# Optimization experiments

Hardware: AMD Instinct MI355X
Metric: run time of the kernel (lower is better)

Reference implementation:

```python
import jax, jax.numpy as jnp
import numpy as np

V, H, B, T = 8192, 1024, 64, 128

def setup_inputs() -> dict:
    key = jax.random.key(0)
    ks = jax.random.split(key, 7)
    s = 1.0 / np.sqrt(H)                     # torch LSTMCell/Linear default init bound
    xg = np.sqrt(6.0 / (H + V))              # xavier_uniform for fc_out.weight
    return {
        "h0":   jax.random.normal(ks[0], (B, H), jnp.float32),
        "W_ih": jax.random.uniform(ks[1], (4 * H, V), jnp.float32, -s, s),
        "W_hh": jax.random.uniform(ks[2], (4 * H, H), jnp.float32, -s, s),
        "b_ih": jax.random.uniform(ks[3], (4 * H,), jnp.float32, -s, s),
        "b_hh": jax.random.uniform(ks[4], (4 * H,), jnp.float32, -s, s),
        "W_fc": jax.random.uniform(ks[5], (V, H), jnp.float32, -xg, xg),
        "b_fc": jax.random.uniform(ks[6], (V,), jnp.float32, -s, s),
        "max_length": T,
    }

def reference(h0, W_ih, W_hh, b_ih, b_hh, W_fc, b_fc, max_length):
    B_, H_ = h0.shape
    V_ = W_ih.shape[1]
    # hidden state fed to the cell is ALWAYS features[1] (h0) in the original code,
    # so its contribution to the gates is constant across timesteps.
    hh = h0 @ W_hh.T + b_hh + b_ih  # (B, 4H)

    def step(carry, _):
        x, c = carry                          # x: (B,V) accumulated one-hots, c: (B,H)
        gates = x @ W_ih.T + hh               # (B, 4H), torch gate order i,f,g,o
        i, f, g, o = jnp.split(gates, 4, axis=1)
        c = jax.nn.sigmoid(f) * c + jax.nn.sigmoid(i) * jnp.tanh(g)
        h = jax.nn.sigmoid(o) * jnp.tanh(c)
        out = h @ W_fc.T + b_fc               # (B, V)
        idx = jnp.argmax(out, axis=1)
        x = x + jax.nn.one_hot(idx, V_, dtype=x.dtype)  # +1 at argmax (cumulative)
        return (x, c), out

    init = (jnp.zeros((B_, V_), h0.dtype), jnp.zeros((B_, H_), h0.dtype))
    _, outs = jax.lax.scan(step, init, None, length=max_length)  # (T, B, V)
    return jnp.transpose(outs, (1, 2, 0))  # (B, V, T)
```

## Files before the change

kernel.cpp:

```cpp
#include <hip/hip_runtime.h>
#include <math.h>

#define VDIM 8192
#define HDIM 1024
#define BDIM 64
#define TDIM 128
#define H4   4096
#define TCH  16
#define NFC  512
#define GS   1088

__device__ __forceinline__ float sigf(float x){ return 1.0f/(1.0f + expf(-x)); }

__device__ __forceinline__ unsigned long long packmax(float v, int vidx){
    unsigned int u = __float_as_uint(v);
    u = (u & 0x80000000u) ? ~u : (u | 0x80000000u);
    return ((unsigned long long)u << 32) | (unsigned int)(VDIM - 1 - vidx);
}

__global__ void __launch_bounds__(256)
hh_kernel(const float* __restrict__ h0, const float* __restrict__ W_hh,
          const float* __restrict__ b_ih, const float* __restrict__ b_hh,
          float* __restrict__ gates)
{
    int blk = blockIdx.x;
    int b = blk >> 4;
    int j = (blk & 15)*256 + threadIdx.x;
    const float* hr = h0 + (size_t)b*HDIM;
    const float* wr = W_hh + (size_t)j*HDIM;
    float s = 0.f;
    for (int k = 0; k < HDIM; k += 4){
        float4 hv = *(const float4*)(hr + k);
        float4 wv = *(const float4*)(wr + k);
        s = fmaf(hv.x, wv.x, s); s = fmaf(hv.y, wv.y, s);
        s = fmaf(hv.z, wv.z, s); s = fmaf(hv.w, wv.w, s);
    }
    gates[(size_t)b*H4 + j] = s + b_ih[j] + b_hh[j];
}

__global__ void __launch_bounds__(256)
cell0_kernel(const float* __restrict__ gates, float* __restrict__ cbuf,
             float* __restrict__ hbuf)
{
    int b = blockIdx.x, u = threadIdx.x*4;
    const float* gb = gates + (size_t)b*H4;
    float4 gi = *(const float4*)(gb + u);
    float4 gf = *(const float4*)(gb + 1024 + u);
    float4 gg = *(const float4*)(gb + 2048 + u);
    float4 go = *(const float4*)(gb + 3072 + u);
    (void)gf;
    float4 c4, h4;
    c4.x = sigf(gi.x)*tanhf(gg.x); c4.y = sigf(gi.y)*tanhf(gg.y);
    c4.z = sigf(gi.z)*tanhf(gg.z); c4.w = sigf(gi.w)*tanhf(gg.w);
    h4.x = sigf(go.x)*tanhf(c4.x); h4.y = sigf(go.y)*tanhf(c4.y);
    h4.z = sigf(go.z)*tanhf(c4.z); h4.w = sigf(go.w)*tanhf(c4.w);
    *(float4*)(cbuf + (size_t)b*HDIM + u) = c4;
    *(float4*)(hbuf + (size_t)b*HDIM + u) = h4;
}

__global__ void __launch_bounds__(256)
tr_kernel(const float* __restrict__ W, float* __restrict__ WT)
{
    __shared__ float tile[64][65];
    const int jb = blockIdx.x * 64;
    const int vb = blockIdx.y * 64;
    const int tx = threadIdx.x & 63;
    const int ty = threadIdx.x >> 6;
    #pragma unroll
    for (int k = 0; k < 64; k += 4)
        tile[ty + k][tx] = W[(size_t)(jb + ty + k)*VDIM + vb + tx];
    __syncthreads();
    #pragma unroll
    for (int k = 0; k < 64; k += 4)
        WT[(size_t)(vb + ty + k)*H4 + jb + tx] = tile[tx][ty + k];
}

__global__ void __launch_bounds__(512, 4)
fc_kernel(const float* __restrict__ W_fc, const float* __restrict__ b_fc,
          const float* __restrict__ hbuf, float* __restrict__ out,
          float* __restrict__ stage,
          unsigned long long* __restrict__ pmax, int t)
{
    __shared__ float buf[16*GS];
    __shared__ unsigned long long bmax[256];
    const int tid = threadIdx.x;
    const int blk = blockIdx.x;
    const int vbase = blk * 16;
    const int g  = tid >> 5;
    const int s  = tid & 31;
    const int b0 = (s >> 2) * 8;
    const int v0 = (s & 3) * 4;
    const int k0 = g * 64;

    float acc[8][4];
    #pragma unroll
    for (int i=0;i<8;++i){
        #pragma unroll
        for (int j=0;j<4;++j) acc[i][j] = 0.f;
    }

    const float* hb = hbuf + (size_t)b0*HDIM + k0;
    const float* wb = W_fc + (size_t)(vbase + v0)*HDIM + k0;

    #pragma unroll 2
    for (int kc = 0; kc < 16; ++kc){
        float4 h4[8], w4[4];
        #pragma unroll
        for (int i=0;i<8;++i) h4[i] = *(const float4*)(hb + (size_t)i*HDIM + kc*4);
        #pragma unroll
        for (int j=0;j<4;++j) w4[j] = *(const float4*)(wb + (size_t)j*HDIM + kc*4);
        #pragma unroll
        for (int i=0;i<8;++i){
            #pragma unroll
            for (int j=0;j<4;++j){
                acc[i][j] = fmaf(h4[i].x, w4[j].x, acc[i][j]);
                acc[i][j] = fmaf(h4[i].y, w4[j].y, acc[i][j]);
                acc[i][j] = fmaf(h4[i].z, w4[j].z, acc[i][j]);
                acc[i][j] = fmaf(h4[i].w, w4[j].w, acc[i][j]);
            }
        }
    }

    {
        float* bp = buf + g*GS;
        #pragma unroll
        for (int i=0;i<8;++i){
            #pragma unroll
            for (int j=0;j<4;++j) bp[(b0+i)*17 + v0 + j] = acc[i][j];
        }
    }
    __syncthreads();

    if (tid < 256){
        const int eb = tid >> 2;
        const int vv = (tid & 3) * 4;
        float4 rr[16];
        #pragma unroll
        for (int q=0;q<16;++q){
            const float* bp = buf + q*GS + eb*17 + vv;
            rr[q].x = bp[0]; rr[q].y = bp[1]; rr[q].z = bp[2]; rr[q].w = bp[3];
        }
        #pragma unroll
        for (int half = 8; half >= 1; half >>= 1){
            #pragma unroll
            for (int i=0;i<8;++i){
                if (i < half){
                    rr[i].x += rr[i+half].x; rr[i].y += rr[i+half].y;
                    rr[i].z += rr[i+half].z; rr[i].w += rr[i+half].w;
                }
            }
        }
        float4 r = rr[0];
        const int v = vbase + vv;
        r.x += b_fc[v]; r.y += b_fc[v+1]; r.z += b_fc[v+2]; r.w += b_fc[v+3];
        if (stage){
            *(float4*)(stage + (((size_t)(t & (TCH-1))*BDIM + eb)*VDIM + v)) = r;
        } else {
            float* ob = out + ((size_t)eb*VDIM + v)*TDIM + t;
            ob[0] = r.x; ob[TDIM] = r.y; ob[2*TDIM] = r.z; ob[3*TDIM] = r.w;
        }
        unsigned long long m  = packmax(r.x, v);
        unsigned long long m2 = packmax(r.y, v+1); if (m2 > m) m = m2;
        m2 = packmax(r.z, v+2); if (m2 > m) m = m2;
        m2 = packmax(r.w, v+3); if (m2 > m) m = m2;
        bmax[tid] = m;
    }
    __syncthreads();
    if (tid < 64){
        unsigned long long mm = bmax[tid*4];
        #pragma unroll
        for (int q=1;q<4;++q){ unsigned long long z = bmax[tid*4+q]; if (z > mm) mm = z; }
        pmax[(size_t)tid*NFC + blk] = mm;
    }
}

__global__ void __launch_bounds__(256)
flush_kernel(const float* __restrict__ stage, float* __restrict__ out, int t0)
{
    const size_t n = (size_t)blockIdx.x*256 + threadIdx.x;
    const int b = (int)(n >> 13);
    const int v = (int)(n & (VDIM-1));
    const size_t st = (size_t)BDIM*VDIM;
    const float* sp = stage + (size_t)b*VDIM + v;
    float* op = out + ((size_t)b*VDIM + v)*TDIM + t0;
    float4 o0, o1, o2, o3;
    o0.x = sp[0*st];  o0.y = sp[1*st];  o0.z = sp[2*st];  o0.w = sp[3*st];
    o1.x = sp[4*st];  o1.y = sp[5*st];  o1.z = sp[6*st];  o1.w = sp[7*st];
    o2.x = sp[8*st];  o2.y = sp[9*st];  o2.z = sp[10*st]; o2.w = sp[11*st];
    o3.x = sp[12*st]; o3.y = sp[13*st]; o3.z = sp[14*st]; o3.w = sp[15*st];
    *(float4*)(op + 0)  = o0;
    *(float4*)(op + 4)  = o1;
    *(float4*)(op + 8)  = o2;
    *(float4*)(op + 12) = o3;
}

__global__ void __launch_bounds__(256)
cell_kernel(const float* __restrict__ W_ih, const float* __restrict__ W_ihT,
            float* __restrict__ gates, float* __restrict__ cbuf,
            float* __restrict__ hbuf, const unsigned long long* __restrict__ pmax)
{
    __shared__ float gbuf[H4];
    __shared__ unsigned long long red[256];
    const int b = blockIdx.x, tid = threadIdx.x;

    {
        unsigned long long a = pmax[(size_t)b*NFC + tid];
        unsigned long long c = pmax[(size_t)b*NFC + tid + 256];
        red[tid] = (c > a) ? c : a;
    }
    __syncthreads();
    for (int st = 128; st; st >>= 1){
        if (tid < st){ if (red[tid+st] > red[tid]) red[tid] = red[tid+st]; }
        __syncthreads();
    }
    const int idx = VDIM - 1 - (int)(unsigned int)(red[0] & 0xffffffffULL);

    float* gb = gates + (size_t)b*H4;
    if (W_ihT){
        const float* row = W_ihT + (size_t)idx*H4;
        #pragma unroll
        for (int q = 0; q < 4; ++q){
            int j4 = q*1024 + tid*4;
            float4 wv = *(const float4*)(row + j4);
            float4 gv = *(const float4*)(gb + j4);
            gv.x += wv.x; gv.y += wv.y; gv.z += wv.z; gv.w += wv.w;
            *(float4*)(gb + j4) = gv;
            *(float4*)(gbuf + j4) = gv;
        }
    } else {
        #pragma unroll
        for (int q = 0; q < 16; ++q){
            int j = q*256 + tid;
            float gv = gb[j] + W_ih[(size_t)j*VDIM + idx];
            gb[j] = gv;
            gbuf[j] = gv;
        }
    }
    __syncthreads();

    int u = tid*4;
    float4 gi = *(float4*)(gbuf + u);
    float4 gf = *(float4*)(gbuf + 1024 + u);
    float4 gg = *(float4*)(gbuf + 2048 + u);
    float4 go = *(float4*)(gbuf + 3072 + u);
    float4 c4 = *(float4*)(cbuf + (size_t)b*HDIM + u);
    c4.x = sigf(gf.x)*c4.x + sigf(gi.x)*tanhf(gg.x);
    c4.y = sigf(gf.y)*c4.y + sigf(gi.y)*tanhf(gg.y);
    c4.z = sigf(gf.z)*c4.z + sigf(gi.z)*tanhf(gg.z);
    c4.w = sigf(gf.w)*c4.w + sigf(gi.w)*tanhf(gg.w);
    float4 h4;
    h4.x = sigf(go.x)*tanhf(c4.x); h4.y = sigf(go.y)*tanhf(c4.y);
    h4.z = sigf(go.z)*tanhf(c4.z); h4.w = sigf(go.w)*tanhf(c4.w);
    *(float4*)(cbuf + (size_t)b*HDIM + u) = c4;
    *(float4*)(hbuf + (size_t)b*HDIM + u) = h4;
}

extern "C" void kernel_launch(void* const* d_in, const int* in_sizes, int n_in,
                              void* d_out, int out_size, void* d_ws, size_t ws_size,
                              hipStream_t stream)
{
    const float* h0   = (const float*)d_in[0];
    const float* W_ih = (const float*)d_in[1];
    const float* W_hh = (const float*)d_in[2];
    const float* b_ih = (const float*)d_in[3];
    const float* b_hh = (const float*)d_in[4];
    const float* W_fc = (const float*)d_in[5];
    const float* b_fc = (const float*)d_in[6];
    float* out = (float*)d_out;

    float* gates = (float*)d_ws;
    float* cbuf  = gates + (size_t)BDIM*H4;
    float* hbuf  = cbuf  + (size_t)BDIM*HDIM;
    unsigned long long* pmax = (unsigned long long*)(hbuf + (size_t)BDIM*HDIM);

    size_t off = (size_t)BDIM*H4*4 + 2*(size_t)BDIM*HDIM*4 + (size_t)BDIM*NFC*8;
    const size_t STAGE_B = (size_t)TCH*BDIM*VDIM*4;
    const size_t WT_B    = (size_t)VDIM*H4*4;
    float* stage = nullptr;
    float* wT    = nullptr;
    if (ws_size >= off + STAGE_B){ stage = (float*)((char*)d_ws + off); off += STAGE_B; }
    if (ws_size >= off + WT_B)   { wT    = (float*)((char*)d_ws + off); off += WT_B; }

    hipLaunchKernelGGL(hh_kernel, dim3(1024), dim3(256), 0, stream,
                       h0, W_hh, b_ih, b_hh, gates);
    hipLaunchKernelGGL(cell0_kernel, dim3(64), dim3(256), 0, stream,
                       gates, cbuf, hbuf);
    if (wT){
        hipLaunchKernelGGL(tr_kernel, dim3(64, 128), dim3(256), 0, stream,
                           W_ih, wT);
    }

    for (int t = 0; t < TDIM; ++t){
        hipLaunchKernelGGL(fc_kernel, dim3(NFC), dim3(512), 0, stream,
                           W_fc, b_fc, hbuf, out, stage, pmax, t);
        if (stage && (t & (TCH-1)) == (TCH-1)){
            hipLaunchKernelGGL(flush_kernel, dim3(BDIM*VDIM/256), dim3(256), 0, stream,
                               stage, out, t - (TCH-1));
        }
        if (t < TDIM - 1){
            hipLaunchKernelGGL(cell_kernel, dim3(64), dim3(256), 0, stream,
                               W_ih, wT, gates, cbuf, hbuf, pmax);
        }
    }
}
```

Measured before the change: 7.987 ms.

## Split FC kernel across batch halves and widen cell kernel grid

The FC kernel now splits the batch into two halves, launching 1024 blocks that each compute 32 batch rows by 16 vocab entries, which halves per-thread register accumulators and doubles grid parallelism. The cell step, when the transposed W_ih is available, becomes a 256-block kernel of single wavefronts. Each block redoes the argmax reduction with wave shuffles and handles a quarter of the hidden units, so no shared memory or block syncs are needed. The trade-off is that h and W tiles are loaded twice across batch halves and the argmax reduction is repeated four times per batch row.

```diff
diff --git a/kernel.cpp b/kernel.cpp
--- a/kernel.cpp
+++ b/kernel.cpp
@@ -8,7 +8,7 @@
 #define H4   4096
 #define TCH  16
 #define NFC  512
-#define GS   1088
+#define GS2  544
 
 __device__ __forceinline__ float sigf(float x){ return 1.0f/(1.0f + expf(-x)); }
 
@@ -81,20 +81,23 @@
           float* __restrict__ stage,
           unsigned long long* __restrict__ pmax, int t)
 {
-    __shared__ float buf[16*GS];
-    __shared__ unsigned long long bmax[256];
+    __shared__ float buf[16*GS2];
+    __shared__ unsigned long long bmax[128];
     const int tid = threadIdx.x;
     const int blk = blockIdx.x;
-    const int vbase = blk * 16;
+    const int bh  = blk >> 9;
+    const int vt  = blk & 511;
+    const int vbase = vt * 16;
     const int g  = tid >> 5;
     const int s  = tid & 31;
-    const int b0 = (s >> 2) * 8;
-    const int v0 = (s & 3) * 4;
-    const int k0 = g * 64;
-
-    float acc[8][4];
-    #pragma unroll
-    for (int i=0;i<8;++i){
+    const int lb0 = (s >> 2) * 4;
+    const int v0  = (s & 3) * 4;
+    const int b0  = bh*32 + lb0;
+    const int k0  = g * 64;
+
+    float acc[4][4];
+    #pragma unroll
+    for (int i=0;i<4;++i){
         #pragma unroll
         for (int j=0;j<4;++j) acc[i][j] = 0.f;
     }
@@ -104,13 +107,13 @@
 
     #pragma unroll 2
     for (int kc = 0; kc < 16; ++kc){
-        float4 h4[8], w4[4];
-        #pragma unroll
-        for (int i=0;i<8;++i) h4[i] = *(const float4*)(hb + (size_t)i*HDIM + kc*4);
+        float4 h4[4], w4[4];
+        #pragma unroll
+        for (int i=0;i<4;++i) h4[i] = *(const float4*)(hb + (size_t)i*HDIM + kc*4);
         #pragma unroll
         for (int j=0;j<4;++j) w4[j] = *(const float4*)(wb + (size_t)j*HDIM + kc*4);
         #pragma unroll
-        for (int i=0;i<8;++i){
+        for (int i=0;i<4;++i){
             #pragma unroll
             for (int j=0;j<4;++j){
                 acc[i][j] = fmaf(h4[i].x, w4[j].x, acc[i][j]);
@@ -122,22 +125,22 @@
     }
 
     {
-        float* bp = buf + g*GS;
-        #pragma unroll
-        for (int i=0;i<8;++i){
+        float* bp = buf + g*GS2;
+        #pragma unroll
+        for (int i=0;i<4;++i){
             #pragma unroll
-            for (int j=0;j<4;++j) bp[(b0+i)*17 + v0 + j] = acc[i][j];
-        }
-    }
-    __syncthreads();
-
-    if (tid < 256){
+            for (int j=0;j<4;++j) bp[(lb0+i)*17 + v0 + j] = acc[i][j];
+        }
+    }
+    __syncthreads();
+
+    if (tid < 128){
         const int eb = tid >> 2;
         const int vv = (tid & 3) * 4;
         float4 rr[16];
         #pragma unroll
         for (int q=0;q<16;++q){
-            const float* bp = buf + q*GS + eb*17 + vv;
+            const float* bp = buf + q*GS2 + eb*17 + vv;
             rr[q].x = bp[0]; rr[q].y = bp[1]; rr[q].z = bp[2]; rr[q].w = bp[3];
         }
         #pragma unroll
@@ -152,11 +155,12 @@
         }
         float4 r = rr[0];
         const int v = vbase + vv;
+        const int b = bh*32 + eb;
         r.x += b_fc[v]; r.y += b_fc[v+1]; r.z += b_fc[v+2]; r.w += b_fc[v+3];
         if (stage){
-            *(float4*)(stage + (((size_t)(t & (TCH-1))*BDIM + eb)*VDIM + v)) = r;
+            *(float4*)(stage + (((size_t)(t & (TCH-1))*BDIM + b)*VDIM + v)) = r;
         } else {
-            float* ob = out + ((size_t)eb*VDIM + v)*TDIM + t;
+            float* ob = out + ((size_t)b*VDIM + v)*TDIM + t;
             ob[0] = r.x; ob[TDIM] = r.y; ob[2*TDIM] = r.z; ob[3*TDIM] = r.w;
         }
         unsigned long long m  = packmax(r.x, v);
@@ -166,11 +170,11 @@
         bmax[tid] = m;
     }
     __syncthreads();
-    if (tid < 64){
+    if (tid < 32){
         unsigned long long mm = bmax[tid*4];
         #pragma unroll
         for (int q=1;q<4;++q){ unsigned long long z = bmax[tid*4+q]; if (z > mm) mm = z; }
-        pmax[(size_t)tid*NFC + blk] = mm;
+        pmax[(size_t)(bh*32 + tid)*NFC + vt] = mm;
     }
 }
 
@@ -194,10 +198,65 @@
     *(float4*)(op + 12) = o3;
 }
 
-__global__ void __launch_bounds__(256)
-cell_kernel(const float* __restrict__ W_ih, const float* __restrict__ W_ihT,
-            float* __restrict__ gates, float* __restrict__ cbuf,
-            float* __restrict__ hbuf, const unsigned long long* __restrict__ pmax)
+__global__ void __launch_bounds__(64)
+cell_kernel(const float* __restrict__ W_ihT, float* __restrict__ gates,
+            float* __restrict__ cbuf, float* __restrict__ hbuf,
+            const unsigned long long* __restrict__ pmax)
+{
+    const int blk = blockIdx.x;
+    const int cb = blk & 63;
+    const int cq = blk >> 6;
+    const int lane = threadIdx.x;
+
+    const unsigned long long* pp = pmax + (size_t)cb*NFC;
+    unsigned long long m = pp[lane];
+    #pragma unroll
+    for (int q = 1; q < 8; ++q){
+        unsigned long long z = pp[q*64 + lane]; if (z > m) m = z;
+    }
+    #pragma unroll
+    for (int d = 32; d >= 1; d >>= 1){
+        unsigned long long z = __shfl_xor(m, d); if (z > m) m = z;
+    }
+    const int idx = VDIM - 1 - (int)(unsigned int)(m & 0xffffffffULL);
+
+    const int u = cq*256 + lane*4;
+    const float* row = W_ihT + (size_t)idx*H4;
+    float* gb = gates + (size_t)cb*H4;
+
+    float4 gi = *(float4*)(gb + u);
+    float4 gf = *(float4*)(gb + 1024 + u);
+    float4 gg = *(float4*)(gb + 2048 + u);
+    float4 go = *(float4*)(gb + 3072 + u);
+    float4 wi = *(const float4*)(row + u);
+    float4 wf = *(const float4*)(row + 1024 + u);
+    float4 wg = *(const float4*)(row + 2048 + u);
+    float4 wo = *(const float4*)(row + 3072 + u);
+    gi.x += wi.x; gi.y += wi.y; gi.z += wi.z; gi.w += wi.w;
+    gf.x += wf.x; gf.y += wf.y; gf.z += wf.z; gf.w += wf.w;
+    gg.x += wg.x; gg.y += wg.y; gg.z += wg.z; gg.w += wg.w;
+    go.x += wo.x; go.y += wo.y; go.z += wo.z; go.w += wo.w;
+    *(float4*)(gb + u)        = gi;
+    *(float4*)(gb + 1024 + u) = gf;
+    *(float4*)(gb + 2048 + u) = gg;
+    *(float4*)(gb + 3072 + u) = go;
+
+    float4 c4 = *(float4*)(cbuf + (size_t)cb*HDIM + u);
+    c4.x = sigf(gf.x)*c4.x + sigf(gi.x)*tanhf(gg.x);
+    c4.y = sigf(gf.y)*c4.y + sigf(gi.y)*tanhf(gg.y);
+    c4.z = sigf(gf.z)*c4.z + sigf(gi.z)*tanhf(gg.z);
+    c4.w = sigf(gf.w)*c4.w + sigf(gi.w)*tanhf(gg.w);
+    float4 h4;
+    h4.x = sigf(go.x)*tanhf(c4.x); h4.y = sigf(go.y)*tanhf(c4.y);
+    h4.z = sigf(go.z)*tanhf(c4.z); h4.w = sigf(go.w)*tanhf(c4.w);
+    *(float4*)(cbuf + (size_t)cb*HDIM + u) = c4;
+    *(float4*)(hbuf + (size_t)cb*HDIM + u) = h4;
+}
+
+__global__ void __launch_bounds__(256)
+cell_fb_kernel(const float* __restrict__ W_ih, float* __restrict__ gates,
+               float* __restrict__ cbuf, float* __restrict__ hbuf,
+               const unsigned long long* __restrict__ pmax)
 {
     __shared__ float gbuf[H4];
     __shared__ unsigned long long red[256];
@@ -216,25 +275,12 @@
     const int idx = VDIM - 1 - (int)(unsigned int)(red[0] & 0xffffffffULL);
 
     float* gb = gates + (size_t)b*H4;
-    if (W_ihT){
-        const float* row = W_ihT + (size_t)idx*H4;
-        #pragma unroll
-        for (int q = 0; q < 4; ++q){
-            int j4 = q*1024 + tid*4;
-            float4 wv = *(const float4*)(row + j4);
-            float4 gv = *(const float4*)(gb + j4);
-            gv.x += wv.x; gv.y += wv.y; gv.z += wv.z; gv.w += wv.w;
-            *(float4*)(gb + j4) = gv;
-            *(float4*)(gbuf + j4) = gv;
-        }
-    } else {
-        #pragma unroll
-        for (int q = 0; q < 16; ++q){
-            int j = q*256 + tid;
-            float gv = gb[j] + W_ih[(size_t)j*VDIM + idx];
-            gb[j] = gv;
-            gbuf[j] = gv;
-        }
+    #pragma unroll
+    for (int q = 0; q < 16; ++q){
+        int j = q*256 + tid;
+        float gv = gb[j] + W_ih[(size_t)j*VDIM + idx];
+        gb[j] = gv;
+        gbuf[j] = gv;
     }
     __syncthreads();
 
@@ -291,15 +337,20 @@
     }
 
     for (int t = 0; t < TDIM; ++t){
-        hipLaunchKernelGGL(fc_kernel, dim3(NFC), dim3(512), 0, stream,
+        hipLaunchKernelGGL(fc_kernel, dim3(1024), dim3(512), 0, stream,
                            W_fc, b_fc, hbuf, out, stage, pmax, t);
         if (stage && (t & (TCH-1)) == (TCH-1)){
             hipLaunchKernelGGL(flush_kernel, dim3(BDIM*VDIM/256), dim3(256), 0, stream,
                                stage, out, t - (TCH-1));
         }
         if (t < TDIM - 1){
-            hipLaunchKernelGGL(cell_kernel, dim3(64), dim3(256), 0, stream,
-                               W_ih, wT, gates, cbuf, hbuf, pmax);
-        }
-    }
-}
+            if (wT){
+                hipLaunchKernelGGL(cell_kernel, dim3(256), dim3(64), 0, stream,
+                                   wT, gates, cbuf, hbuf, pmax);
+            } else {
+                hipLaunchKernelGGL(cell_fb_kernel, dim3(64), dim3(256), 0, stream,
+                                   W_ih, gates, cbuf, hbuf, pmax);
+            }
+        }
+    }
+}
```

Result: slower. 11.04 ms (+38.3%).
